# Kernel optimization log

Hardware: AMD Instinct MI355X
Metric: run time of the kernel (lower is better)

Reference implementation:

```python
import jax, jax.numpy as jnp
import numpy as np

B, C, H, W = 8, 128, 64, 64


def setup_inputs() -> dict:
    key = jax.random.key(0)
    ks = jax.random.split(key, 8)
    s = 1.0 / np.sqrt(C)
    return {
        "x1": jax.random.normal(ks[0], (B, C, H, W), dtype=jnp.float32),
        "x2": jax.random.normal(ks[1], (B, C, H, W), dtype=jnp.float32),
        "Wq": jax.random.normal(ks[2], (C, C), dtype=jnp.float32) * s,
        "bq": jax.random.normal(ks[3], (C,), dtype=jnp.float32) * s,
        "Wk": jax.random.normal(ks[4], (C, C), dtype=jnp.float32) * s,
        "bk": jax.random.normal(ks[5], (C,), dtype=jnp.float32) * s,
        "Wv": jax.random.normal(ks[6], (C, C), dtype=jnp.float32) * s,
        "bv": jax.random.normal(ks[7], (C,), dtype=jnp.float32) * s,
    }


def reference(x1, x2, Wq, bq, Wk, bk, Wv, bv):
    b, c, h, w = x1.shape
    n = h * w
    # 1x1 conv == channel matmul per pixel; flatten spatial dims -> [b, c, n]
    x1f = x1.reshape(b, c, n)
    x2f = x2.reshape(b, c, n)
    q = jnp.einsum("oc,bcn->bno", Wq, x1f) + bq[None, None, :]  # [b, n, c]
    k = jnp.einsum("oc,bcn->bon", Wk, x2f) + bk[None, :, None]  # [b, c, n]
    v = jnp.einsum("oc,bcn->bon", Wv, x2f) + bv[None, :, None]  # [b, c, n]
    energy = jnp.einsum("bnc,bcm->bnm", q, k)                   # [b, n, n] (unscaled)
    attention = jax.nn.softmax(energy, axis=-1)
    # out[b,c,i] = sum_j v[b,c,j] * attention[b,i,j]
    out = jnp.einsum("bcj,bij->bci", v, attention)
    return out.reshape(b, c, h, w)
```

## Files before the change

kernel.cpp:

```cpp
#include <hip/hip_runtime.h>

typedef float f4 __attribute__((ext_vector_type(4)));
typedef float f16v __attribute__((ext_vector_type(16)));
typedef _Float16 hf;
typedef __fp16 fp16x2 __attribute__((ext_vector_type(2)));
typedef hf h8 __attribute__((ext_vector_type(8)));
typedef unsigned short ushort_t;
typedef unsigned int uint_t;
typedef uint_t u4 __attribute__((ext_vector_type(4)));

#define BATCH 8
#define CH 128
#define NPIX 4096
#define LOG2E 1.4426950408889634f
#define XSTR 65

__device__ inline f16v mfma32h(h8 a, h8 b, f16v c) {
    return __builtin_amdgcn_mfma_f32_32x32x16_f16(a, b, c, 0, 0, 0);
}

__device__ inline uint_t pk2h(float a, float b) {
    fp16x2 pp = __builtin_amdgcn_cvt_pkrtz(a, b);
    union { fp16x2 v; uint_t u; } cv;
    cv.v = pp;
    return cv.u;
}

typedef __attribute__((address_space(3))) uint_t lds_uint;
typedef __attribute__((address_space(1))) const uint_t global_uint;
__device__ inline void dma16(const void* g, void* l) {
    __builtin_amdgcn_global_load_lds((global_uint*)g, (lds_uint*)l, 16, 0, 0);
}

__global__ __launch_bounds__(256) void wprep_kernel(const float* __restrict__ Wq,
                                                    const float* __restrict__ Wk,
                                                    const float* __restrict__ Wv,
                                                    hf* __restrict__ WqT, hf* __restrict__ WkT,
                                                    hf* __restrict__ Wv16) {
    int m = blockIdx.x;
    const float* W = (m == 0) ? Wq : (m == 1) ? Wk : Wv;
    float s = (m == 0) ? LOG2E : 1.0f;
    for (int idx = threadIdx.x; idx < CH * CH; idx += 256) {
        int o = idx >> 7, c = idx & 127;
        float v = W[idx] * s;
        if (m == 0) WqT[c * CH + o] = (hf)v;
        else if (m == 1) WkT[c * CH + o] = (hf)v;
        else Wv16[idx] = (hf)v;
    }
}

__global__ __launch_bounds__(256) void qkv_kernel(const float* __restrict__ x1,
                                                  const float* __restrict__ x2,
                                                  const hf* __restrict__ WqT,
                                                  const hf* __restrict__ WkT,
                                                  const hf* __restrict__ Wv16,
                                                  const float* __restrict__ bq,
                                                  const float* __restrict__ bk,
                                                  const float* __restrict__ bv,
                                                  hf* __restrict__ Qf, hf* __restrict__ Kf,
                                                  hf* __restrict__ Vf) {
    __shared__ __align__(16) float Xs[CH * XSTR];

    int bid = blockIdx.x;
    int m = bid >> 9;
    int rem = bid & 511;
    int b = rem & 7;
    int n0 = (rem >> 3) << 6;

    const float* X = ((m == 0) ? x1 : x2) + (size_t)b * CH * NPIX;
    const float* bias = (m == 0) ? bq : (m == 1) ? bk : bv;

    int tid = threadIdx.x;
#pragma unroll
    for (int r = 0; r < 8; ++r) {
        int c = 16 * r + (tid >> 4);
        int n4 = (tid & 15) << 2;
        f4 v = *(const f4*)&X[(size_t)c * NPIX + n0 + n4];
#pragma unroll
        for (int j = 0; j < 4; ++j) Xs[c * XSTR + n4 + j] = v[j];
    }
    __syncthreads();

    int lane = tid & 63;
    int w = tid >> 6;
    int h = lane >> 5;
    int m32 = lane & 31;
    int o0 = w * 32;

    h8 wf[8];
    if (m == 2) {
#pragma unroll
        for (int kc = 0; kc < 8; ++kc)
            wf[kc] = *(const h8*)&Wv16[(size_t)(o0 + m32) * CH + kc * 16 + h * 8];
    } else {
        const hf* WT = (m == 0) ? WqT : WkT;
#pragma unroll
        for (int kc = 0; kc < 8; ++kc) {
            h8 t;
#pragma unroll
            for (int j = 0; j < 8; ++j) t[j] = WT[(size_t)(kc * 16 + h * 8 + j) * CH + o0 + m32];
            wf[kc] = t;
        }
    }

    f16v acc[2];
#pragma unroll
    for (int g = 0; g < 2; ++g)
#pragma unroll
        for (int r = 0; r < 16; ++r) acc[g][r] = 0.f;

#pragma unroll
    for (int g = 0; g < 2; ++g) {
        const float* xbase = &Xs[h * 8 * XSTR + g * 32 + m32];
#pragma unroll
        for (int kc = 0; kc < 8; ++kc) {
            h8 xh, xl;
#pragma unroll
            for (int j = 0; j < 8; ++j) {
                float f = xbase[(kc * 16 + j) * XSTR];
                hf hi = (hf)f;
                xh[j] = hi;
                xl[j] = (hf)(f - (float)hi);
            }
            if (m == 2) {
                acc[g] = mfma32h(wf[kc], xh, acc[g]);
                acc[g] = mfma32h(wf[kc], xl, acc[g]);
            } else {
                acc[g] = mfma32h(xh, wf[kc], acc[g]);
                acc[g] = mfma32h(xl, wf[kc], acc[g]);
            }
        }
    }

    if (m < 2) {
        float bval = bias[o0 + m32] * ((m == 0) ? LOG2E : 1.0f);
        hf* Y = ((m == 0) ? Qf : Kf) + (size_t)b * NPIX * CH;
#pragma unroll
        for (int g = 0; g < 2; ++g)
#pragma unroll
            for (int r = 0; r < 16; ++r) {
                int n = n0 + g * 32 + (r & 3) + 8 * (r >> 2) + 4 * h;
                Y[(size_t)n * CH + o0 + m32] = (hf)(acc[g][r] + bval);
            }
    } else {
        hf* Yv = Vf + (size_t)b * CH * NPIX;
#pragma unroll
        for (int g = 0; g < 2; ++g)
#pragma unroll
            for (int r = 0; r < 16; ++r) {
                int o = o0 + (r & 3) + 8 * (r >> 2) + 4 * h;
                Yv[(size_t)o * NPIX + n0 + g * 32 + m32] = (hf)(acc[g][r] + bias[o]);
            }
    }
}

__global__ __launch_bounds__(256, 2) void attn_kernel(const hf* __restrict__ Qf,
                                                      const hf* __restrict__ Kf,
                                                      const hf* __restrict__ Vf,
                                                      hf* __restrict__ Opart,
                                                      float* __restrict__ Mpart,
                                                      float* __restrict__ Lpart) {
    __shared__ __align__(16) ushort_t smem[32768];

    int tid = threadIdx.x;
    int lane = tid & 63;
    int w = tid >> 6;
    int h = lane >> 5;
    int m32 = lane & 31;
    int qh = w >> 1, kh = w & 1;

    int idx = blockIdx.x;
    int b = idx & 7;
    int ks = (idx >> 3) & 1;
    int qt = idx >> 4;
    int i0g = qt << 7;
    int k0g = ks << 11;
    int krow = kh * 32 + m32;

    const hf* Qb = Qf + (size_t)b * NPIX * CH;
    const hf* Kb = Kf + (size_t)b * NPIX * CH;
    const hf* Vb = Vf + (size_t)b * CH * NPIX;

    h8 qf[2][8];
#pragma unroll
    for (int g = 0; g < 2; ++g) {
        size_t row = (size_t)(i0g + qh * 64 + g * 32 + m32) * CH + h * 8;
#pragma unroll
        for (int kc = 0; kc < 8; ++kc) qf[g][kc] = *(const h8*)&Qb[row + kc * 16];
    }

    const hf* pK[4];
    const hf* pV[4];
#pragma unroll
    for (int a = 0; a < 4; ++a) {
        int g = w * 4 + a;
        int rowk = g * 4 + (lane >> 4);
        int lck = (lane & 15) ^ (rowk & 15);
        pK[a] = Kb + (size_t)(k0g + rowk) * CH + lck * 8;
        int rowv = g * 8 + (lane >> 3);
        int lcv = (lane & 7) ^ (rowv & 7);
        pV[a] = Vb + (size_t)rowv * NPIX + k0g + lcv * 8;
    }

#pragma unroll
    for (int a = 0; a < 4; ++a) {
        dma16(pK[a], &smem[(w * 4 + a) * 512]);
        dma16(pV[a], &smem[16384 + (w * 4 + a) * 512]);
        pK[a] += 64 * CH;
        pV[a] += 64;
    }

    f16v accO[2][4];
#pragma unroll
    for (int g = 0; g < 2; ++g)
#pragma unroll
        for (int ct = 0; ct < 4; ++ct)
#pragma unroll
            for (int r = 0; r < 16; ++r) accO[g][ct][r] = 0.f;
    float mprev[2] = {-1e30f, -1e30f};
    float lsum[2] = {0.f, 0.f};

    int pc2s[2];
#pragma unroll
    for (int g2 = 0; g2 < 2; ++g2) pc2s[g2] = (kh * 4 + g2 * 2 + h) ^ (m32 & 7);

    __syncthreads();

    for (int t = 0; t < 32; ++t) {
        int cur = t & 1;
        if (t < 31) {
            int nb = 1 - cur;
#pragma unroll
            for (int a = 0; a < 4; ++a) {
                dma16(pK[a], &smem[nb * 8192 + (w * 4 + a) * 512]);
                dma16(pV[a], &smem[16384 + nb * 8192 + (w * 4 + a) * 512]);
                pK[a] += 64 * CH;
                pV[a] += 64;
            }
        }
        const ushort_t* kb = smem + cur * 8192;
        const ushort_t* vb = smem + 16384 + cur * 8192;

        f16v acc0, acc1;
#pragma unroll
        for (int r = 0; r < 16; ++r) { acc0[r] = 0.f; acc1[r] = 0.f; }
#pragma unroll
        for (int kc = 0; kc < 8; ++kc) {
            int pA = (kc * 2 + h) ^ (m32 & 15);
            h8 ahi = *(const h8*)&kb[krow * 128 + pA * 8];
            acc0 = mfma32h(ahi, qf[0][kc], acc0);
            acc1 = mfma32h(ahi, qf[1][kc], acc1);
        }

        h8 pbp[2][2];
#pragma unroll
        for (int g = 0; g < 2; ++g) {
            f16v& acc = g ? acc1 : acc0;
            float m1 = fmaxf(fmaxf(acc[0], acc[1]), fmaxf(acc[2], acc[3]));
            float m2 = fmaxf(fmaxf(acc[4], acc[5]), fmaxf(acc[6], acc[7]));
            float m3 = fmaxf(fmaxf(acc[8], acc[9]), fmaxf(acc[10], acc[11]));
            float m4 = fmaxf(fmaxf(acc[12], acc[13]), fmaxf(acc[14], acc[15]));
            float tmax = fmaxf(fmaxf(m1, m2), fmaxf(m3, m4));
            tmax = fmaxf(tmax, __shfl_xor(tmax, 32));
            if (__any(tmax > mprev[g])) {
                float mnew = fmaxf(mprev[g], tmax);
                float alpha = exp2f(mprev[g] - mnew);
                lsum[g] *= alpha;
#pragma unroll
                for (int ct = 0; ct < 4; ++ct)
#pragma unroll
                    for (int r = 0; r < 16; ++r) accO[g][ct][r] *= alpha;
                mprev[g] = mnew;
            }

            float p[16];
#pragma unroll
            for (int r = 0; r < 16; ++r) p[r] = exp2f(acc[r] - mprev[g]);
            float ps[8];
#pragma unroll
            for (int r = 0; r < 8; ++r) ps[r] = p[r] + p[r + 8];
#pragma unroll
            for (int r = 0; r < 4; ++r) ps[r] += ps[r + 4];
            float psum = (ps[0] + ps[1]) + (ps[2] + ps[3]);
            psum += __shfl_xor(psum, 32);
            lsum[g] += psum;

            uint_t pk[8], rv[8];
#pragma unroll
            for (int t2 = 0; t2 < 8; ++t2) pk[t2] = pk2h(p[2 * t2], p[2 * t2 + 1]);
#pragma unroll
            for (int t2 = 0; t2 < 8; ++t2) rv[t2] = (uint_t)__shfl_xor((int)pk[t2], 32);
#pragma unroll
            for (int g2 = 0; g2 < 2; ++g2) {
                u4 fv;
                fv[0] = h ? rv[g2 * 4 + 2] : pk[g2 * 4 + 0];
                fv[1] = h ? rv[g2 * 4 + 3] : pk[g2 * 4 + 1];
                fv[2] = h ? pk[g2 * 4 + 2] : rv[g2 * 4 + 0];
                fv[3] = h ? pk[g2 * 4 + 3] : rv[g2 * 4 + 1];
                __builtin_memcpy(&pbp[g][g2], &fv, 16);
            }
        }

#pragma unroll
        for (int g2 = 0; g2 < 2; ++g2) {
            int pc2 = pc2s[g2];
#pragma unroll
            for (int ct = 0; ct < 4; ++ct) {
                h8 av = *(const h8*)&vb[(ct * 32 + m32) * 64 + pc2 * 8];
                accO[0][ct] = mfma32h(av, pbp[0][g2], accO[0][ct]);
                accO[1][ct] = mfma32h(av, pbp[1][g2], accO[1][ct]);
            }
        }

        __syncthreads();
    }

    float* scr = (float*)smem;
    if (h == 0) {
#pragma unroll
        for (int g = 0; g < 2; ++g) {
            scr[kh * 128 + qh * 64 + g * 32 + m32] = mprev[g];
            scr[256 + kh * 128 + qh * 64 + g * 32 + m32] = lsum[g];
        }
    }
    __syncthreads();
    float fk[2], Mv[2], Lv[2];
#pragma unroll
    for (int g = 0; g < 2; ++g) {
        float mo = scr[(1 - kh) * 128 + qh * 64 + g * 32 + m32];
        float lo2 = scr[256 + (1 - kh) * 128 + qh * 64 + g * 32 + m32];
        float M = fmaxf(mprev[g], mo);
        fk[g] = exp2f(mprev[g] - M);
        float fo = exp2f(mo - M);
        Mv[g] = M;
        Lv[g] = lsum[g] * fk[g] + lo2 * fo;
    }
    __syncthreads();

    float* mrg = (float*)smem;
    if (kh == 1) {
#pragma unroll
        for (int g = 0; g < 2; ++g)
#pragma unroll
            for (int ct = 0; ct < 4; ++ct)
#pragma unroll
                for (int r = 0; r < 16; ++r) {
                    int ch = ct * 32 + (r & 3) + 8 * (r >> 2) + 4 * h;
                    mrg[ch * 128 + qh * 64 + g * 32 + m32] = accO[g][ct][r] * fk[g];
                }
    }
    __syncthreads();
    if (kh == 0) {
        size_t base = (((size_t)ks * 8 + b) * 32 + qt) * 16384;
        size_t mlb = (((size_t)ks * 8 + b) * 32 + qt) * 128;
#pragma unroll
        for (int g = 0; g < 2; ++g) {
            int q = qh * 64 + g * 32 + m32;
#pragma unroll
            for (int ct = 0; ct < 4; ++ct)
#pragma unroll
                for (int r = 0; r < 16; ++r) {
                    int ch = ct * 32 + (r & 3) + 8 * (r >> 2) + 4 * h;
                    Opart[base + ch * 128 + q] = (hf)(accO[g][ct][r] * fk[g] + mrg[ch * 128 + q]);
                }
            if (h == 0) {
                Mpart[mlb + q] = Mv[g];
                Lpart[mlb + q] = Lv[g];
            }
        }
    }
}

__global__ __launch_bounds__(256) void combine_kernel(const hf* __restrict__ Opart,
                                                      const float* __restrict__ Mp,
                                                      const float* __restrict__ Lp,
                                                      float* __restrict__ out) {
    int idx = blockIdx.x;
    int b = idx & 7;
    int qt = idx >> 3;
    int tid = threadIdx.x;
    int q = tid & 127;
    int ch0 = (tid >> 7) << 6;

    size_t base0 = (((size_t)b) * 32 + qt) * 16384;
    size_t base1 = ((((size_t)8 + b)) * 32 + qt) * 16384;
    size_t ml0 = (((size_t)b) * 32 + qt) * 128 + q;
    size_t ml1 = ((((size_t)8 + b)) * 32 + qt) * 128 + q;

    float M0 = Mp[ml0], M1 = Mp[ml1];
    float L0 = Lp[ml0], L1 = Lp[ml1];
    float M = fmaxf(M0, M1);
    float w0 = exp2f(M0 - M), w1 = exp2f(M1 - M);
    float rd = 1.0f / (w0 * L0 + w1 * L1);

    float* O = out + (size_t)b * CH * NPIX + ((size_t)qt << 7);
#pragma unroll 4
    for (int c = ch0; c < ch0 + 64; ++c) {
        float o0 = (float)Opart[base0 + c * 128 + q];
        float o1 = (float)Opart[base1 + c * 128 + q];
        O[(size_t)c * NPIX + q] = (w0 * o0 + w1 * o1) * rd;
    }
}

extern "C" void kernel_launch(void* const* d_in, const int* in_sizes, int n_in,
                              void* d_out, int out_size, void* d_ws, size_t ws_size,
                              hipStream_t stream) {
    const float* x1 = (const float*)d_in[0];
    const float* x2 = (const float*)d_in[1];
    const float* Wq = (const float*)d_in[2];
    const float* bq = (const float*)d_in[3];
    const float* Wk = (const float*)d_in[4];
    const float* bk = (const float*)d_in[5];
    const float* Wv = (const float*)d_in[6];
    const float* bv = (const float*)d_in[7];
    float* outp = (float*)d_out;

    const size_t N = (size_t)BATCH * NPIX * CH;
    hf* Qf = (hf*)d_ws;
    hf* Kf = Qf + N;
    hf* Vf = Qf + 2 * N;
    hf* WqT = Qf + 3 * N;
    hf* WkT = WqT + CH * CH;
    hf* Wv16 = WqT + 2 * CH * CH;
    hf* Opart = WqT + 3 * CH * CH;
    float* Mp = (float*)(Opart + (size_t)2 * 8 * 32 * 16384);
    float* Lp = Mp + (size_t)2 * 8 * 32 * 128;

    wprep_kernel<<<3, 256, 0, stream>>>(Wq, Wk, Wv, WqT, WkT, Wv16);
    qkv_kernel<<<3 * BATCH * (NPIX / 64), 256, 0, stream>>>(x1, x2, WqT, WkT, Wv16,
                                                            bq, bk, bv, Qf, Kf, Vf);
    attn_kernel<<<BATCH * 2 * (NPIX / 128), 256, 0, stream>>>(Qf, Kf, Vf, Opart, Mp, Lp);
    combine_kernel<<<BATCH * (NPIX / 128), 256, 0, stream>>>(Opart, Mp, Lp, outp);
}
```

Before: 243.7 us.

## Use permlane32 swap, lazy softmax rescale threshold, and MFMA priority hints

Replaces the eight cross-half shuffles and selects used to build the P operand with four v_permlane32_swap instructions. Softmax rescaling of the output accumulators now happens only when the running max grows by more than a threshold, which skips most rescale passes. The max reduction is reordered into two chains, and s_setprio brackets the MFMA blocks so waves issuing matrix work get scheduling priority. The lazy rescale lets the exp2 arguments go positive, up to about 2^8, which is safe in fp16 and fp32 but changes numerics slightly.

```diff
diff --git a/kernel.cpp b/kernel.cpp
--- a/kernel.cpp
+++ b/kernel.cpp
@@ -14,6 +14,7 @@
 #define NPIX 4096
 #define LOG2E 1.4426950408889634f
 #define XSTR 65
+#define RESCALE_THR 8.0f
 
 __device__ inline f16v mfma32h(h8 a, h8 b, f16v c) {
     return __builtin_amdgcn_mfma_f32_32x32x16_f16(a, b, c, 0, 0, 0);
@@ -24,6 +25,10 @@
     union { fp16x2 v; uint_t u; } cv;
     cv.v = pp;
     return cv.u;
+}
+
+__device__ inline void pl32swap(uint_t& a, uint_t& b) {
+    asm("v_permlane32_swap_b32 %0, %1" : "+v"(a), "+v"(b));
 }
 
 typedef __attribute__((address_space(3))) uint_t lds_uint;
@@ -244,6 +249,7 @@
         f16v acc0, acc1;
 #pragma unroll
         for (int r = 0; r < 16; ++r) { acc0[r] = 0.f; acc1[r] = 0.f; }
+        __builtin_amdgcn_s_setprio(1);
 #pragma unroll
         for (int kc = 0; kc < 8; ++kc) {
             int pA = (kc * 2 + h) ^ (m32 & 15);
@@ -251,18 +257,22 @@
             acc0 = mfma32h(ahi, qf[0][kc], acc0);
             acc1 = mfma32h(ahi, qf[1][kc], acc1);
         }
+        __builtin_amdgcn_s_setprio(0);
 
         h8 pbp[2][2];
 #pragma unroll
         for (int g = 0; g < 2; ++g) {
             f16v& acc = g ? acc1 : acc0;
-            float m1 = fmaxf(fmaxf(acc[0], acc[1]), fmaxf(acc[2], acc[3]));
-            float m2 = fmaxf(fmaxf(acc[4], acc[5]), fmaxf(acc[6], acc[7]));
-            float m3 = fmaxf(fmaxf(acc[8], acc[9]), fmaxf(acc[10], acc[11]));
-            float m4 = fmaxf(fmaxf(acc[12], acc[13]), fmaxf(acc[14], acc[15]));
-            float tmax = fmaxf(fmaxf(m1, m2), fmaxf(m3, m4));
+            float ta = fmaxf(fmaxf(acc[0], acc[1]), acc[2]);
+            float tb = fmaxf(fmaxf(acc[3], acc[4]), acc[5]);
+            ta = fmaxf(fmaxf(ta, acc[6]), acc[7]);
+            tb = fmaxf(fmaxf(tb, acc[8]), acc[9]);
+            ta = fmaxf(fmaxf(ta, acc[10]), acc[11]);
+            tb = fmaxf(fmaxf(tb, acc[12]), acc[13]);
+            ta = fmaxf(fmaxf(ta, acc[14]), acc[15]);
+            float tmax = fmaxf(ta, tb);
             tmax = fmaxf(tmax, __shfl_xor(tmax, 32));
-            if (__any(tmax > mprev[g])) {
+            if (__any(tmax > mprev[g] + RESCALE_THR)) {
                 float mnew = fmaxf(mprev[g], tmax);
                 float alpha = exp2f(mprev[g] - mnew);
                 lsum[g] *= alpha;
@@ -285,22 +295,25 @@
             psum += __shfl_xor(psum, 32);
             lsum[g] += psum;
 
-            uint_t pk[8], rv[8];
+            uint_t pk[8];
 #pragma unroll
             for (int t2 = 0; t2 < 8; ++t2) pk[t2] = pk2h(p[2 * t2], p[2 * t2 + 1]);
-#pragma unroll
-            for (int t2 = 0; t2 < 8; ++t2) rv[t2] = (uint_t)__shfl_xor((int)pk[t2], 32);
+            pl32swap(pk[0], pk[2]);
+            pl32swap(pk[1], pk[3]);
+            pl32swap(pk[4], pk[6]);
+            pl32swap(pk[5], pk[7]);
 #pragma unroll
             for (int g2 = 0; g2 < 2; ++g2) {
                 u4 fv;
-                fv[0] = h ? rv[g2 * 4 + 2] : pk[g2 * 4 + 0];
-                fv[1] = h ? rv[g2 * 4 + 3] : pk[g2 * 4 + 1];
-                fv[2] = h ? pk[g2 * 4 + 2] : rv[g2 * 4 + 0];
-                fv[3] = h ? pk[g2 * 4 + 3] : rv[g2 * 4 + 1];
+                fv[0] = pk[g2 * 4 + 0];
+                fv[1] = pk[g2 * 4 + 1];
+                fv[2] = pk[g2 * 4 + 2];
+                fv[3] = pk[g2 * 4 + 3];
                 __builtin_memcpy(&pbp[g][g2], &fv, 16);
             }
         }
 
+        __builtin_amdgcn_s_setprio(1);
 #pragma unroll
         for (int g2 = 0; g2 < 2; ++g2) {
             int pc2 = pc2s[g2];
@@ -311,6 +324,7 @@
                 accO[1][ct] = mfma32h(av, pbp[1][g2], accO[1][ct]);
             }
         }
+        __builtin_amdgcn_s_setprio(0);
 
         __syncthreads();
     }
```

Result: faster. 237.1 us (-2.7%).
